# Performance work log

Hardware: AMD Instinct MI355X
Metric: run time of the kernel (lower is better)

The kernel has to match this reference:

```python
import jax, jax.numpy as jnp
import numpy as np
from jax.scipy.linalg import expm

DIM = 128
BF = 2          # branching_factor
H = 8           # num_heads
MAX_DEPTH = 12
PAD = BF + 1    # padding value used by pad_sequence in the torch module
N = 256         # number of positions


def setup_inputs() -> dict:
    key = jax.random.key(0)
    k1, k2 = jax.random.split(key)
    # raw _primitives parameter (the torch init applies softmax+cumsum to rand;
    # any values work for the math -- only the skew-hermitian part matters)
    prim = jax.random.uniform(k1, (BF * H + 1, DIM, DIM), dtype=jnp.float32)
    positions = jax.random.randint(k2, (N,), 0, BF ** MAX_DEPTH)  # node indices, >= 0
    return {"primitives_param": prim, "positions": positions}


def _path_words(positions):
    """Vectorized equivalent of create_paths + pad_sequence.

    For node index n the branch path is built by walking up the tree:
    branch = (n-1) % BF, parent = (n-1) // BF. Digits come out leaf->root,
    so we reverse the valid prefix and right-pad with PAD to MAX_DEPTH.
    """
    d = positions.astype(jnp.int32)
    digs = []
    for _ in range(MAX_DEPTH):
        valid = d > 0
        digs.append(jnp.where(valid, (d - 1) % BF, PAD))
        d = jnp.where(valid, (d - 1) // BF, 0)
    R = jnp.stack(digs, axis=1)            # (N, 12) leaf->root digits
    depth = jnp.sum(R != PAD, axis=1)       # path length per token
    idx = depth[:, None] - 1 - jnp.arange(MAX_DEPTH)[None, :]
    pw = jnp.take_along_axis(R, jnp.clip(idx, 0, MAX_DEPTH - 1), axis=1)
    pw = jnp.where(idx >= 0, pw, PAD)       # (N, 12) root->leaf, PAD-padded
    return pw, depth


def reference(primitives_param, positions):
    pw, depth = _path_words(positions)

    # ---- steps matrix (tree distance), mirrors the no_grad block ----
    pm = pw != PAD                                        # (N, 12)
    mask = pm[:, None, :] & pm[None, :, :]                # (N, N, 12)
    eq = pw[:, None, :] == pw[None, :, :]
    common = jnp.cumprod(eq.astype(jnp.int32), axis=-1).astype(bool) & mask
    cpl = common.sum(-1)                                  # common prefix length
    steps = depth[:, None] + depth[None, :] - 2 * cpl     # (N, N) int

    # ---- unitary primitives: expm of the skew(-hermitian, real) part ----
    skew = primitives_param - jnp.swapaxes(primitives_param, -1, -2)
    prims = expm(skew)                                    # (BF*H+1, DIM, DIM)
    sos = prims[-1]
    P = prims[:-1].reshape(BF, H, DIM, DIM)

    n_tok = pw.shape[0]
    maps = jnp.broadcast_to(jnp.eye(DIM, dtype=prims.dtype)[None, None],
                            (n_tok, H, DIM, DIM))
    sos_ptr = pw[:, 0] == -1                              # never true for pos>=0, kept for fidelity
    maps = jnp.where(sos_ptr[:, None, None, None], sos[None, None], maps)

    # fused gather-indexed scan over tree depth: instead of BF masked matmuls
    # per depth, gather each token's branch primitive and do one batched matmul.
    for d in range(MAX_DEPTH):
        sel = pw[:, d]                                    # (N,) in {0..BF-1} or PAD
        Pk = P[jnp.clip(sel, 0, BF - 1)]                  # (N, H, DIM, DIM)
        new = jnp.einsum('nhij,nhjk->nhik', maps, Pk)
        maps = jnp.where((sel < BF)[:, None, None, None], new, maps)

    return maps, steps
```

## Files before the change

### kernel.cpp

```cpp
#include <hip/hip_runtime.h>

typedef unsigned short ushort_t;
typedef unsigned int uint_t;
typedef __attribute__((ext_vector_type(8))) short bf16x8;
typedef __attribute__((ext_vector_type(4))) float f32x4;

#define NMAT 16
#define MSZ 16384
#define NTAB 126

__device__ __forceinline__ ushort_t f32_bf16(float f) {
  uint_t u = __builtin_bit_cast(uint_t, f);
  u += 0x7FFFu + ((u >> 16) & 1u);
  return (ushort_t)(u >> 16);
}

__device__ __forceinline__ float bf16_f32(ushort_t b) {
  uint_t u = ((uint_t)b) << 16;
  return __builtin_bit_cast(float, u);
}

__device__ __forceinline__ int swz(int r, int k) {
  return r * 128 + (((k >> 3) ^ (r & 7)) << 3) + (k & 7);
}

__device__ __forceinline__ int tab_off(int L) { return (1 << L) - 2; }

__device__ __forceinline__ void mm_frag(const ushort_t* U, const ushort_t* V,
                                        int r0, int c0, int quad, int l16,
                                        f32x4 (&acc)[4][4]) {
#pragma unroll
  for (int rt = 0; rt < 4; rt++)
#pragma unroll
    for (int ct = 0; ct < 4; ct++) {
      f32x4 z = {0.f, 0.f, 0.f, 0.f};
      acc[rt][ct] = z;
    }
#pragma unroll
  for (int kt = 0; kt < 4; kt++) {
    int k = kt * 32 + quad * 8;
    bf16x8 a[4], b[4];
#pragma unroll
    for (int rt = 0; rt < 4; rt++) a[rt] = *(const bf16x8*)(&U[swz(r0 + rt * 16 + l16, k)]);
#pragma unroll
    for (int ct = 0; ct < 4; ct++) b[ct] = *(const bf16x8*)(&V[swz(c0 + ct * 16 + l16, k)]);
#pragma unroll
    for (int rt = 0; rt < 4; rt++)
#pragma unroll
      for (int ct = 0; ct < 4; ct++)
        acc[rt][ct] = __builtin_amdgcn_mfma_f32_16x16x32_bf16(a[rt], b[ct], acc[rt][ct], 0, 0, 0);
  }
}

__device__ __forceinline__ void store_T(ushort_t* dst, const f32x4 (&acc)[4][4],
                                        int r0, int c0, int quad, int l16,
                                        float scale, float cdiag) {
#pragma unroll
  for (int rt = 0; rt < 4; rt++)
#pragma unroll
    for (int ct = 0; ct < 4; ct++) {
      int dr = r0 + rt * 16 + quad * 4, dc = c0 + ct * 16 + l16;
      float v[4];
#pragma unroll
      for (int i = 0; i < 4; i++) {
        v[i] = scale * acc[rt][ct][i];
        if (dr + i == dc) v[i] += cdiag;
      }
      uint2 pk;
      pk.x = (uint_t)f32_bf16(v[0]) | ((uint_t)f32_bf16(v[1]) << 16);
      pk.y = (uint_t)f32_bf16(v[2]) | ((uint_t)f32_bf16(v[3]) << 16);
      *(uint2*)(&dst[swz(dc, dr)]) = pk;
    }
}

__device__ __forceinline__ void set_ident(ushort_t* dst, int t, float c) {
  ushort_t cb = f32_bf16(c);
  for (int i = 0; i < 64; i++) {
    int e = i * 256 + t;
    int r = e >> 7, k = e & 127;
    dst[swz(r, k)] = (r == k) ? cb : (ushort_t)0;
  }
}

__global__ __launch_bounds__(256, 1) void expm1_kernel(const float* __restrict__ prim,
                                                       ushort_t* __restrict__ wsCS) {
  __shared__ ushort_t __align__(16) bufA[MSZ];
  __shared__ ushort_t __align__(16) bufB[MSZ];
  int kmat = blockIdx.x >> 1, which = blockIdx.x & 1;
  int t = threadIdx.x, wave = t >> 6, lane = t & 63;
  int quad = lane >> 4, l16 = lane & 15;
  int r0 = (wave >> 1) * 64, c0 = (wave & 1) * 64;
  const float* p = prim + kmat * MSZ;

  for (int i = 0; i < 64; i++) {
    int e = i * 256 + t;
    int r = e >> 7, c = e & 127;
    bufA[swz(r, c)] = f32_bf16((p[r * 128 + c] - p[c * 128 + r]) * 0.125f);
  }
  __syncthreads();

  f32x4 acc[4][4];
  mm_frag(bufA, bufA, r0, c0, quad, l16, acc);
  __syncthreads();
  store_T(bufB, acc, r0, c0, quad, l16, -1.f, 0.f);
  __syncthreads();

  uint2 yv[4][4];
#pragma unroll
  for (int rt = 0; rt < 4; rt++)
#pragma unroll
    for (int ct = 0; ct < 4; ct++) {
      int dr = r0 + rt * 16 + quad * 4, dc = c0 + ct * 16 + l16;
      yv[rt][ct] = *(const uint2*)(&bufB[swz(dc, dr)]);
    }

  mm_frag(bufB, bufB, r0, c0, quad, l16, acc);
  __syncthreads();
  store_T(bufB, acc, r0, c0, quad, l16, 1.f, 0.f);

  float coef[9];
  if (which == 0) {
    coef[0] = 1.f; coef[1] = 1.f / 2; coef[2] = 1.f / 24; coef[3] = 1.f / 720;
    coef[4] = 1.f / 40320; coef[5] = 1.f / 3628800.f; coef[6] = 1.f / 479001600.f;
    coef[7] = 1.f / 87178291200.f; coef[8] = 1.f / 20922789888000.f;
  } else {
    coef[0] = 1.f; coef[1] = 1.f / 6; coef[2] = 1.f / 120; coef[3] = 1.f / 5040;
    coef[4] = 1.f / 362880.f; coef[5] = 1.f / 39916800.f; coef[6] = 1.f / 6227020800.f;
    coef[7] = 1.f / 1307674368000.f; coef[8] = 1.f / 355687428096000.f;
  }

  set_ident(bufA, t, coef[8]);
  __syncthreads();

#pragma unroll
  for (int k = 3; k >= 0; k--) {
    mm_frag(bufB, bufA, r0, c0, quad, l16, acc);
    __syncthreads();
    float cd = coef[2 * k], cy = coef[2 * k + 1];
#pragma unroll
    for (int rt = 0; rt < 4; rt++)
#pragma unroll
      for (int ct = 0; ct < 4; ct++) {
        int dr = r0 + rt * 16 + quad * 4, dc = c0 + ct * 16 + l16;
        uint2 yp = yv[rt][ct];
        float y[4] = {bf16_f32((ushort_t)(yp.x & 0xffff)), bf16_f32((ushort_t)(yp.x >> 16)),
                      bf16_f32((ushort_t)(yp.y & 0xffff)), bf16_f32((ushort_t)(yp.y >> 16))};
        float v[4];
#pragma unroll
        for (int i = 0; i < 4; i++) {
          v[i] = acc[rt][ct][i] + cy * y[i];
          if (dr + i == dc) v[i] += cd;
        }
        uint2 pk;
        pk.x = (uint_t)f32_bf16(v[0]) | ((uint_t)f32_bf16(v[1]) << 16);
        pk.y = (uint_t)f32_bf16(v[2]) | ((uint_t)f32_bf16(v[3]) << 16);
        *(uint2*)(&bufA[swz(dc, dr)]) = pk;
      }
    __syncthreads();
  }
  ushort_t* dst = wsCS + (size_t)(which * NMAT + kmat) * MSZ;
  for (int i = 0; i < 8; i++) {
    int e = (i * 256 + t) * 8;
    int r = e >> 7, k = e & 127;
    *(uint4*)(dst + e) = *(const uint4*)(&bufA[swz(r, k)]);
  }
}

__global__ __launch_bounds__(256, 1) void expm2_kernel(
    const float* __restrict__ prim, const ushort_t* __restrict__ wsCS,
    ushort_t* __restrict__ TN, ushort_t* __restrict__ TT) {
  __shared__ ushort_t __align__(16) bufA[MSZ];
  __shared__ ushort_t __align__(16) bufB[MSZ];
  int kmat = blockIdx.x;
  int t = threadIdx.x, wave = t >> 6, lane = t & 63;
  int quad = lane >> 4, l16 = lane & 15;
  int r0 = (wave >> 1) * 64, c0 = (wave & 1) * 64;
  const float* p = prim + kmat * MSZ;
  const ushort_t* Cg = wsCS + (size_t)kmat * MSZ;
  const ushort_t* Sg = wsCS + (size_t)(NMAT + kmat) * MSZ;

  for (int i = 0; i < 64; i++) {
    int e = i * 256 + t;
    int r = e >> 7, c = e & 127;
    bufA[swz(r, c)] = f32_bf16((p[r * 128 + c] - p[c * 128 + r]) * 0.125f);
  }
  for (int i = 0; i < 8; i++) {
    int e = (i * 256 + t) * 8;
    int r = e >> 7, k = e & 127;
    *(uint4*)(&bufB[swz(r, k)]) = *(const uint4*)(Sg + e);
  }
  __syncthreads();

  f32x4 acc[4][4];
  mm_frag(bufA, bufB, r0, c0, quad, l16, acc);
  __syncthreads();
#pragma unroll
  for (int rt = 0; rt < 4; rt++)
#pragma unroll
    for (int ct = 0; ct < 4; ct++) {
      int dr = r0 + rt * 16 + quad * 4, dc = c0 + ct * 16 + l16;
      uint2 cp = *(const uint2*)(Cg + dc * 128 + dr);
      float cf[4] = {bf16_f32((ushort_t)(cp.x & 0xffff)), bf16_f32((ushort_t)(cp.x >> 16)),
                     bf16_f32((ushort_t)(cp.y & 0xffff)), bf16_f32((ushort_t)(cp.y >> 16))};
      uint2 en, et;
      en.x = (uint_t)f32_bf16(cf[0] - acc[rt][ct][0]) | ((uint_t)f32_bf16(cf[1] - acc[rt][ct][1]) << 16);
      en.y = (uint_t)f32_bf16(cf[2] - acc[rt][ct][2]) | ((uint_t)f32_bf16(cf[3] - acc[rt][ct][3]) << 16);
      et.x = (uint_t)f32_bf16(cf[0] + acc[rt][ct][0]) | ((uint_t)f32_bf16(cf[1] + acc[rt][ct][1]) << 16);
      et.y = (uint_t)f32_bf16(cf[2] + acc[rt][ct][2]) | ((uint_t)f32_bf16(cf[3] + acc[rt][ct][3]) << 16);
      *(uint2*)(&bufA[swz(dc, dr)]) = en;
      *(uint2*)(&bufB[swz(dc, dr)]) = et;
    }
  __syncthreads();

#pragma unroll 1
  for (int sq = 0; sq < 3; sq++) {
    mm_frag(bufA, bufB, r0, c0, quad, l16, acc);
    __syncthreads();
#pragma unroll
    for (int rt = 0; rt < 4; rt++)
#pragma unroll
      for (int ct = 0; ct < 4; ct++) {
        int dr = r0 + rt * 16 + quad * 4, dc = c0 + ct * 16 + l16;
        uint2 pk;
        pk.x = (uint_t)f32_bf16(acc[rt][ct][0]) | ((uint_t)f32_bf16(acc[rt][ct][1]) << 16);
        pk.y = (uint_t)f32_bf16(acc[rt][ct][2]) | ((uint_t)f32_bf16(acc[rt][ct][3]) << 16);
        *(uint2*)(&bufB[swz(dc, dr)]) = pk;
#pragma unroll
        for (int i = 0; i < 4; i++) bufA[swz(dr + i, dc)] = f32_bf16(acc[rt][ct][i]);
      }
    __syncthreads();
  }
  for (int i = 0; i < 8; i++) {
    int e = (i * 256 + t) * 8;
    int r = e >> 7, k = e & 127;
    *(uint4*)(TN + (size_t)kmat * MSZ + e) = *(const uint4*)(&bufA[swz(r, k)]);
    *(uint4*)(TT + (size_t)kmat * MSZ + e) = *(const uint4*)(&bufB[swz(r, k)]);
  }
}

__global__ __launch_bounds__(256) void table_kernel(ushort_t* __restrict__ TN,
                                                    ushort_t* __restrict__ TT, int mode) {
  int bx = blockIdx.x;
  int eA, eB, eO, h;
  if (mode == 0) {
    int c = bx >> 3; h = bx & 7;
    eA = c >> 1; eB = c & 1; eO = 2 + c;
  } else if (mode == 1) {
    if (bx < 64) {
      int c = bx >> 3; h = bx & 7;
      eA = 2 + (c >> 1); eB = c & 1; eO = 6 + c;
    } else {
      int c = (bx - 64) >> 3; h = (bx - 64) & 7;
      eA = 2 + (c >> 2); eB = 2 + (c & 3); eO = 14 + c;
    }
  } else {
    if (bx < 256) {
      int c = bx >> 3; h = bx & 7;
      eA = 2 + (c >> 3); eB = 6 + (c & 7); eO = 30 + c;
    } else {
      int c = (bx - 256) >> 3; h = (bx - 256) & 7;
      eA = 6 + (c >> 3); eB = 6 + (c & 7); eO = 62 + c;
    }
  }
  int t = threadIdx.x, wave = t >> 6, lane = t & 63;
  int quad = lane >> 4, l16 = lane & 15;
  int r0 = (wave >> 1) * 64, c0 = (wave & 1) * 64;
  const ushort_t* A = TN + ((size_t)eA * 8 + h) * MSZ;
  const ushort_t* B = TT + ((size_t)eB * 8 + h) * MSZ;
  ushort_t* oN = TN + ((size_t)eO * 8 + h) * MSZ;
  ushort_t* oT = TT + ((size_t)eO * 8 + h) * MSZ;

  f32x4 acc[4][4];
#pragma unroll
  for (int rt = 0; rt < 4; rt++)
#pragma unroll
    for (int ct = 0; ct < 4; ct++) {
      f32x4 z = {0.f, 0.f, 0.f, 0.f};
      acc[rt][ct] = z;
    }
#pragma unroll
  for (int kt = 0; kt < 4; kt++) {
    bf16x8 a[4], b[4];
#pragma unroll
    for (int rt = 0; rt < 4; rt++)
      a[rt] = *(const bf16x8*)(A + (r0 + rt * 16 + l16) * 128 + kt * 32 + quad * 8);
#pragma unroll
    for (int ct = 0; ct < 4; ct++)
      b[ct] = *(const bf16x8*)(B + (c0 + ct * 16 + l16) * 128 + kt * 32 + quad * 8);
#pragma unroll
    for (int rt = 0; rt < 4; rt++)
#pragma unroll
      for (int ct = 0; ct < 4; ct++)
        acc[rt][ct] = __builtin_amdgcn_mfma_f32_16x16x32_bf16(a[rt], b[ct], acc[rt][ct], 0, 0, 0);
  }
#pragma unroll
  for (int rt = 0; rt < 4; rt++)
#pragma unroll
    for (int ct = 0; ct < 4; ct++) {
      int dr = r0 + rt * 16 + quad * 4, dc = c0 + ct * 16 + l16;
      uint2 pk;
      pk.x = (uint_t)f32_bf16(acc[rt][ct][0]) | ((uint_t)f32_bf16(acc[rt][ct][1]) << 16);
      pk.y = (uint_t)f32_bf16(acc[rt][ct][2]) | ((uint_t)f32_bf16(acc[rt][ct][3]) << 16);
      *(uint2*)(oT + dc * 128 + dr) = pk;
#pragma unroll
      for (int i = 0; i < 4; i++) oN[(dr + i) * 128 + dc] = f32_bf16(acc[rt][ct][i]);
    }
}

__global__ void steps_kernel(const int* __restrict__ pos, float* __restrict__ os, int N) {
  int i = blockIdx.x, j = threadIdx.x;
  int mi = pos[i] + 1, mj = pos[j] + 1;
  int di = 31 - __builtin_clz((unsigned)mi);
  int dj = 31 - __builtin_clz((unsigned)mj);
  int tt = di < dj ? di : dj;
  unsigned x = (unsigned)((mi >> (di - tt)) ^ (mj >> (dj - tt)));
  int cpl = tt - (x ? (32 - __builtin_clz(x)) : 0);
  os[i * N + j] = (float)(di + dj - 2 * cpl);
}

__global__ __launch_bounds__(256) void maps_kernel(
    const ushort_t* __restrict__ TN, const ushort_t* __restrict__ TT,
    const int* __restrict__ positions, float* __restrict__ out) {
  int bx = blockIdx.x;
  int n = bx >> 3, h = bx & 7;
  int t = threadIdx.x, wave = t >> 6, lane = t & 63;
  int quad = lane >> 4, l16 = lane & 15;
  int m = positions[n] + 1;
  int depth = 31 - __builtin_clz((unsigned)m);
  float* ob = out + (size_t)(n * 8 + h) * MSZ;

  if (depth == 0) {
    for (int i = 0; i < 64; i++) {
      int e = i * 256 + t;
      int r = e >> 7, k = e & 127;
      ob[e] = (r == k) ? 1.0f : 0.0f;
    }
    return;
  }
  if (depth <= 6) {
    int c = m & ((1 << depth) - 1);
    const ushort_t* src = TN + ((size_t)(tab_off(depth) + c) * 8 + h) * MSZ;
    for (int i = 0; i < 8; i++) {
      int e = (i * 256 + t) * 8;
      bf16x8 v = *(const bf16x8*)(src + e);
      f32x4 lo = {bf16_f32((ushort_t)v[0]), bf16_f32((ushort_t)v[1]),
                  bf16_f32((ushort_t)v[2]), bf16_f32((ushort_t)v[3])};
      f32x4 hi = {bf16_f32((ushort_t)v[4]), bf16_f32((ushort_t)v[5]),
                  bf16_f32((ushort_t)v[6]), bf16_f32((ushort_t)v[7])};
      *(f32x4*)(ob + e) = lo;
      *(f32x4*)(ob + e + 4) = hi;
    }
    return;
  }

  int L0 = depth - 6;
  int c0v = (m >> 6) & ((1 << L0) - 1);
  int suf = m & 63;
  const ushort_t* U = TT + ((size_t)(62 + suf) * 8 + h) * MSZ;
  const ushort_t* V = TN + ((size_t)(tab_off(L0) + c0v) * 8 + h) * MSZ;

  int r0 = (wave >> 1) * 64, c0 = (wave & 1) * 64;
  f32x4 acc[4][4];
#pragma unroll
  for (int rt = 0; rt < 4; rt++)
#pragma unroll
    for (int ct = 0; ct < 4; ct++) {
      f32x4 z = {0.f, 0.f, 0.f, 0.f};
      acc[rt][ct] = z;
    }
#pragma unroll
  for (int kt = 0; kt < 4; kt++) {
    bf16x8 a[4], b[4];
#pragma unroll
    for (int rt = 0; rt < 4; rt++)
      a[rt] = *(const bf16x8*)(U + (r0 + rt * 16 + l16) * 128 + kt * 32 + quad * 8);
#pragma unroll
    for (int ct = 0; ct < 4; ct++)
      b[ct] = *(const bf16x8*)(V + (c0 + ct * 16 + l16) * 128 + kt * 32 + quad * 8);
#pragma unroll
    for (int rt = 0; rt < 4; rt++)
#pragma unroll
      for (int ct = 0; ct < 4; ct++)
        acc[rt][ct] = __builtin_amdgcn_mfma_f32_16x16x32_bf16(a[rt], b[ct], acc[rt][ct], 0, 0, 0);
  }
#pragma unroll
  for (int rt = 0; rt < 4; rt++)
#pragma unroll
    for (int ct = 0; ct < 4; ct++) {
      int dr = r0 + rt * 16 + quad * 4;
      int dc = c0 + ct * 16 + l16;
      *(f32x4*)(ob + dc * 128 + dr) = acc[rt][ct];
    }
}

extern "C" void kernel_launch(void* const* d_in, const int* in_sizes, int n_in,
                              void* d_out, int out_size, void* d_ws, size_t ws_size,
                              hipStream_t stream) {
  const float* prim = (const float*)d_in[0];
  const int* positions = (const int*)d_in[1];
  int N = in_sizes[1];
  float* out = (float*)d_out;

  ushort_t* wsCS = (ushort_t*)d_ws;
  ushort_t* TN = wsCS + (size_t)2 * NMAT * MSZ;
  ushort_t* TT = TN + (size_t)NTAB * 8 * MSZ;

  steps_kernel<<<N, N, 0, stream>>>(positions, out + (size_t)N * 8 * MSZ, N);
  expm1_kernel<<<2 * NMAT, 256, 0, stream>>>(prim, wsCS);
  expm2_kernel<<<NMAT, 256, 0, stream>>>(prim, wsCS, TN, TT);
  table_kernel<<<32, 256, 0, stream>>>(TN, TT, 0);
  table_kernel<<<192, 256, 0, stream>>>(TN, TT, 1);
  table_kernel<<<768, 256, 0, stream>>>(TN, TT, 2);
  maps_kernel<<<N * 8, 256, 0, stream>>>(TN, TT, positions, out);
}
```

Measured before the change: 242.2 us.

## Fuse steps into expm1, stage skew via LDS, restructure table build into two launches

The steps computation now runs as extra blocks of the expm1 launch. expm1 stages the input in LDS and builds the scaled skew matrix with coalesced reads instead of strided transposed global reads. It also writes the skew matrix to a workspace so expm2 can load it instead of recomputing it. The three table launches become two: tableA builds depth-2 and depth-3 entries inside one block through an LDS intermediate, and tableB builds the rest. Each table entry is now formed by two matmuls that write transposed-packed stores, rather than one matmul with scalar strided stores. The changes aim to cut launch count and uncoalesced memory traffic, at the cost of doubling the MFMA work in the table kernels.

```diff
diff --git a/kernel.cpp b/kernel.cpp
--- a/kernel.cpp
+++ b/kernel.cpp
@@ -26,16 +26,20 @@
 
 __device__ __forceinline__ int tab_off(int L) { return (1 << L) - 2; }
 
+__device__ __forceinline__ void mm_zero(f32x4 (&acc)[4][4]) {
+#pragma unroll
+  for (int rt = 0; rt < 4; rt++)
+#pragma unroll
+    for (int ct = 0; ct < 4; ct++) {
+      f32x4 z = {0.f, 0.f, 0.f, 0.f};
+      acc[rt][ct] = z;
+    }
+}
+
 __device__ __forceinline__ void mm_frag(const ushort_t* U, const ushort_t* V,
                                         int r0, int c0, int quad, int l16,
                                         f32x4 (&acc)[4][4]) {
-#pragma unroll
-  for (int rt = 0; rt < 4; rt++)
-#pragma unroll
-    for (int ct = 0; ct < 4; ct++) {
-      f32x4 z = {0.f, 0.f, 0.f, 0.f};
-      acc[rt][ct] = z;
-    }
+  mm_zero(acc);
 #pragma unroll
   for (int kt = 0; kt < 4; kt++) {
     int k = kt * 32 + quad * 8;
@@ -50,6 +54,80 @@
       for (int ct = 0; ct < 4; ct++)
         acc[rt][ct] = __builtin_amdgcn_mfma_f32_16x16x32_bf16(a[rt], b[ct], acc[rt][ct], 0, 0, 0);
   }
+}
+
+__device__ __forceinline__ void mm_gg(const ushort_t* gU, const ushort_t* gV,
+                                      int r0, int c0, int quad, int l16,
+                                      f32x4 (&acc)[4][4]) {
+  mm_zero(acc);
+#pragma unroll
+  for (int kt = 0; kt < 4; kt++) {
+    int k = kt * 32 + quad * 8;
+    bf16x8 a[4], b[4];
+#pragma unroll
+    for (int rt = 0; rt < 4; rt++) a[rt] = *(const bf16x8*)(gU + (r0 + rt * 16 + l16) * 128 + k);
+#pragma unroll
+    for (int ct = 0; ct < 4; ct++) b[ct] = *(const bf16x8*)(gV + (c0 + ct * 16 + l16) * 128 + k);
+#pragma unroll
+    for (int rt = 0; rt < 4; rt++)
+#pragma unroll
+      for (int ct = 0; ct < 4; ct++)
+        acc[rt][ct] = __builtin_amdgcn_mfma_f32_16x16x32_bf16(a[rt], b[ct], acc[rt][ct], 0, 0, 0);
+  }
+}
+
+__device__ __forceinline__ void mm_gl(const ushort_t* gU, const ushort_t* lV,
+                                      int r0, int c0, int quad, int l16,
+                                      f32x4 (&acc)[4][4]) {
+  mm_zero(acc);
+#pragma unroll
+  for (int kt = 0; kt < 4; kt++) {
+    int k = kt * 32 + quad * 8;
+    bf16x8 a[4], b[4];
+#pragma unroll
+    for (int rt = 0; rt < 4; rt++) a[rt] = *(const bf16x8*)(gU + (r0 + rt * 16 + l16) * 128 + k);
+#pragma unroll
+    for (int ct = 0; ct < 4; ct++) b[ct] = *(const bf16x8*)(&lV[swz(c0 + ct * 16 + l16, k)]);
+#pragma unroll
+    for (int rt = 0; rt < 4; rt++)
+#pragma unroll
+      for (int ct = 0; ct < 4; ct++)
+        acc[rt][ct] = __builtin_amdgcn_mfma_f32_16x16x32_bf16(a[rt], b[ct], acc[rt][ct], 0, 0, 0);
+  }
+}
+
+__device__ __forceinline__ void mm_lg(const ushort_t* lU, const ushort_t* gV,
+                                      int r0, int c0, int quad, int l16,
+                                      f32x4 (&acc)[4][4]) {
+  mm_zero(acc);
+#pragma unroll
+  for (int kt = 0; kt < 4; kt++) {
+    int k = kt * 32 + quad * 8;
+    bf16x8 a[4], b[4];
+#pragma unroll
+    for (int rt = 0; rt < 4; rt++) a[rt] = *(const bf16x8*)(&lU[swz(r0 + rt * 16 + l16, k)]);
+#pragma unroll
+    for (int ct = 0; ct < 4; ct++) b[ct] = *(const bf16x8*)(gV + (c0 + ct * 16 + l16) * 128 + k);
+#pragma unroll
+    for (int rt = 0; rt < 4; rt++)
+#pragma unroll
+      for (int ct = 0; ct < 4; ct++)
+        acc[rt][ct] = __builtin_amdgcn_mfma_f32_16x16x32_bf16(a[rt], b[ct], acc[rt][ct], 0, 0, 0);
+  }
+}
+
+__device__ __forceinline__ void store_pk_global(ushort_t* dst, const f32x4 (&acc)[4][4],
+                                                int r0, int c0, int quad, int l16) {
+#pragma unroll
+  for (int rt = 0; rt < 4; rt++)
+#pragma unroll
+    for (int ct = 0; ct < 4; ct++) {
+      int dr = r0 + rt * 16 + quad * 4, dc = c0 + ct * 16 + l16;
+      uint2 pk;
+      pk.x = (uint_t)f32_bf16(acc[rt][ct][0]) | ((uint_t)f32_bf16(acc[rt][ct][1]) << 16);
+      pk.y = (uint_t)f32_bf16(acc[rt][ct][2]) | ((uint_t)f32_bf16(acc[rt][ct][3]) << 16);
+      *(uint2*)(dst + dc * 128 + dr) = pk;
+    }
 }
 
 __device__ __forceinline__ void store_T(ushort_t* dst, const f32x4 (&acc)[4][4],
@@ -82,12 +160,31 @@
   }
 }
 
-__global__ __launch_bounds__(256, 1) void expm1_kernel(const float* __restrict__ prim,
-                                                       ushort_t* __restrict__ wsCS) {
-  __shared__ ushort_t __align__(16) bufA[MSZ];
-  __shared__ ushort_t __align__(16) bufB[MSZ];
-  int kmat = blockIdx.x >> 1, which = blockIdx.x & 1;
-  int t = threadIdx.x, wave = t >> 6, lane = t & 63;
+__global__ __launch_bounds__(256, 2) void expm1_kernel(
+    const float* __restrict__ prim, ushort_t* __restrict__ wsCS,
+    ushort_t* __restrict__ wsX, const int* __restrict__ pos,
+    float* __restrict__ os, int N) {
+  int bx = blockIdx.x;
+  int t = threadIdx.x;
+  if (bx >= 32) {
+    int i = bx - 32, j = t;
+    int mi = pos[i] + 1, mj = pos[j] + 1;
+    int di = 31 - __builtin_clz((unsigned)mi);
+    int dj = 31 - __builtin_clz((unsigned)mj);
+    int tt = di < dj ? di : dj;
+    unsigned x = (unsigned)((mi >> (di - tt)) ^ (mj >> (dj - tt)));
+    int cpl = tt - (x ? (32 - __builtin_clz(x)) : 0);
+    os[i * N + j] = (float)(di + dj - 2 * cpl);
+    return;
+  }
+
+  __shared__ ushort_t __align__(16) smem[2 * MSZ];
+  ushort_t* bufA = smem;
+  ushort_t* bufB = smem + MSZ;
+  float* pf = (float*)smem;
+
+  int kmat = bx >> 1, which = bx & 1;
+  int wave = t >> 6, lane = t & 63;
   int quad = lane >> 4, l16 = lane & 15;
   int r0 = (wave >> 1) * 64, c0 = (wave & 1) * 64;
   const float* p = prim + kmat * MSZ;
@@ -95,7 +192,30 @@
   for (int i = 0; i < 64; i++) {
     int e = i * 256 + t;
     int r = e >> 7, c = e & 127;
-    bufA[swz(r, c)] = f32_bf16((p[r * 128 + c] - p[c * 128 + r]) * 0.125f);
+    pf[r * 128 + (c ^ (r & 31))] = p[e];
+  }
+  __syncthreads();
+
+  ushort_t xr[64];
+#pragma unroll
+  for (int i = 0; i < 64; i++) {
+    int e = i * 256 + t;
+    int r = e >> 7, c = e & 127;
+    float a = pf[r * 128 + (c ^ (r & 31))];
+    float b = pf[c * 128 + (r ^ (c & 31))];
+    xr[i] = f32_bf16((a - b) * 0.125f);
+  }
+  __syncthreads();
+#pragma unroll
+  for (int i = 0; i < 64; i++) {
+    int e = i * 256 + t;
+    int r = e >> 7, c = e & 127;
+    bufA[swz(r, c)] = xr[i];
+  }
+  if (which == 0) {
+    ushort_t* xd = wsX + (size_t)kmat * MSZ;
+#pragma unroll
+    for (int i = 0; i < 64; i++) xd[i * 256 + t] = xr[i];
   }
   __syncthreads();
 
@@ -167,7 +287,7 @@
 }
 
 __global__ __launch_bounds__(256, 1) void expm2_kernel(
-    const float* __restrict__ prim, const ushort_t* __restrict__ wsCS,
+    const ushort_t* __restrict__ wsX, const ushort_t* __restrict__ wsCS,
     ushort_t* __restrict__ TN, ushort_t* __restrict__ TT) {
   __shared__ ushort_t __align__(16) bufA[MSZ];
   __shared__ ushort_t __align__(16) bufB[MSZ];
@@ -175,18 +295,14 @@
   int t = threadIdx.x, wave = t >> 6, lane = t & 63;
   int quad = lane >> 4, l16 = lane & 15;
   int r0 = (wave >> 1) * 64, c0 = (wave & 1) * 64;
-  const float* p = prim + kmat * MSZ;
+  const ushort_t* Xg = wsX + (size_t)kmat * MSZ;
   const ushort_t* Cg = wsCS + (size_t)kmat * MSZ;
   const ushort_t* Sg = wsCS + (size_t)(NMAT + kmat) * MSZ;
 
-  for (int i = 0; i < 64; i++) {
-    int e = i * 256 + t;
-    int r = e >> 7, c = e & 127;
-    bufA[swz(r, c)] = f32_bf16((p[r * 128 + c] - p[c * 128 + r]) * 0.125f);
-  }
   for (int i = 0; i < 8; i++) {
     int e = (i * 256 + t) * 8;
     int r = e >> 7, k = e & 127;
+    *(uint4*)(&bufA[swz(r, k)]) = *(const uint4*)(Xg + e);
     *(uint4*)(&bufB[swz(r, k)]) = *(const uint4*)(Sg + e);
   }
   __syncthreads();
@@ -238,84 +354,79 @@
   }
 }
 
-__global__ __launch_bounds__(256) void table_kernel(ushort_t* __restrict__ TN,
-                                                    ushort_t* __restrict__ TT, int mode) {
+__global__ __launch_bounds__(256, 2) void tableA_kernel(ushort_t* __restrict__ TN,
+                                                        ushort_t* __restrict__ TT) {
+  __shared__ ushort_t __align__(16) Mb[MSZ];
   int bx = blockIdx.x;
-  int eA, eB, eO, h;
-  if (mode == 0) {
-    int c = bx >> 3; h = bx & 7;
-    eA = c >> 1; eB = c & 1; eO = 2 + c;
-  } else if (mode == 1) {
-    if (bx < 64) {
-      int c = bx >> 3; h = bx & 7;
-      eA = 2 + (c >> 1); eB = c & 1; eO = 6 + c;
-    } else {
-      int c = (bx - 64) >> 3; h = (bx - 64) & 7;
-      eA = 2 + (c >> 2); eB = 2 + (c & 3); eO = 14 + c;
-    }
-  } else {
-    if (bx < 256) {
-      int c = bx >> 3; h = bx & 7;
-      eA = 2 + (c >> 3); eB = 6 + (c & 7); eO = 30 + c;
-    } else {
-      int c = (bx - 256) >> 3; h = (bx - 256) & 7;
-      eA = 6 + (c >> 3); eB = 6 + (c & 7); eO = 62 + c;
-    }
-  }
+  int idx = bx >> 3, h = bx & 7;
   int t = threadIdx.x, wave = t >> 6, lane = t & 63;
   int quad = lane >> 4, l16 = lane & 15;
   int r0 = (wave >> 1) * 64, c0 = (wave & 1) * 64;
-  const ushort_t* A = TN + ((size_t)eA * 8 + h) * MSZ;
-  const ushort_t* B = TT + ((size_t)eB * 8 + h) * MSZ;
+
+  int b0, bmid, blast, eO, nmid;
+  if (idx < 4) {
+    int c = idx;
+    b0 = c >> 1; blast = c & 1; bmid = 0; nmid = 0; eO = 2 + c;
+  } else {
+    int c = idx - 4;
+    b0 = c >> 2; bmid = (c >> 1) & 1; blast = c & 1; nmid = 1; eO = 6 + c;
+  }
+
+  {
+    const ushort_t* src = TN + ((size_t)b0 * 8 + h) * MSZ;
+#pragma unroll
+    for (int i = 0; i < 8; i++) {
+      int e = (i * 256 + t) * 8;
+      int r = e >> 7, k = e & 127;
+      *(uint4*)(&Mb[swz(r, k)]) = *(const uint4*)(src + e);
+    }
+  }
+  __syncthreads();
+
+  f32x4 acc[4][4];
+  if (nmid) {
+    const ushort_t* Pt = TT + ((size_t)bmid * 8 + h) * MSZ;
+    mm_gl(Pt, Mb, r0, c0, quad, l16, acc);
+    __syncthreads();
+    store_T(Mb, acc, r0, c0, quad, l16, 1.f, 0.f);
+    __syncthreads();
+  }
+
+  const ushort_t* Pt = TT + ((size_t)blast * 8 + h) * MSZ;
   ushort_t* oN = TN + ((size_t)eO * 8 + h) * MSZ;
   ushort_t* oT = TT + ((size_t)eO * 8 + h) * MSZ;
+  mm_gl(Pt, Mb, r0, c0, quad, l16, acc);
+  store_pk_global(oN, acc, r0, c0, quad, l16);
+  mm_lg(Mb, Pt, r0, c0, quad, l16, acc);
+  store_pk_global(oT, acc, r0, c0, quad, l16);
+}
+
+__global__ __launch_bounds__(256) void tableB_kernel(ushort_t* __restrict__ TN,
+                                                     ushort_t* __restrict__ TT) {
+  int bx = blockIdx.x;
+  int idx = bx >> 3, h = bx & 7;
+  int t = threadIdx.x, wave = t >> 6, lane = t & 63;
+  int quad = lane >> 4, l16 = lane & 15;
+  int r0 = (wave >> 1) * 64, c0 = (wave & 1) * 64;
+
+  int eA, eB, eO;
+  if (idx < 16) {
+    int c = idx;      eA = 2 + (c >> 2); eB = 2 + (c & 3); eO = 14 + c;
+  } else if (idx < 48) {
+    int c = idx - 16; eA = 2 + (c >> 3); eB = 6 + (c & 7); eO = 30 + c;
+  } else {
+    int c = idx - 48; eA = 6 + (c >> 3); eB = 6 + (c & 7); eO = 62 + c;
+  }
+  const ushort_t* An = TN + ((size_t)eA * 8 + h) * MSZ;
+  const ushort_t* Bt = TT + ((size_t)eB * 8 + h) * MSZ;
+  ushort_t* oN = TN + ((size_t)eO * 8 + h) * MSZ;
+  ushort_t* oT = TT + ((size_t)eO * 8 + h) * MSZ;
 
   f32x4 acc[4][4];
-#pragma unroll
-  for (int rt = 0; rt < 4; rt++)
-#pragma unroll
-    for (int ct = 0; ct < 4; ct++) {
-      f32x4 z = {0.f, 0.f, 0.f, 0.f};
-      acc[rt][ct] = z;
-    }
-#pragma unroll
-  for (int kt = 0; kt < 4; kt++) {
-    bf16x8 a[4], b[4];
-#pragma unroll
-    for (int rt = 0; rt < 4; rt++)
-      a[rt] = *(const bf16x8*)(A + (r0 + rt * 16 + l16) * 128 + kt * 32 + quad * 8);
-#pragma unroll
-    for (int ct = 0; ct < 4; ct++)
-      b[ct] = *(const bf16x8*)(B + (c0 + ct * 16 + l16) * 128 + kt * 32 + quad * 8);
-#pragma unroll
-    for (int rt = 0; rt < 4; rt++)
-#pragma unroll
-      for (int ct = 0; ct < 4; ct++)
-        acc[rt][ct] = __builtin_amdgcn_mfma_f32_16x16x32_bf16(a[rt], b[ct], acc[rt][ct], 0, 0, 0);
-  }
-#pragma unroll
-  for (int rt = 0; rt < 4; rt++)
-#pragma unroll
-    for (int ct = 0; ct < 4; ct++) {
-      int dr = r0 + rt * 16 + quad * 4, dc = c0 + ct * 16 + l16;
-      uint2 pk;
-      pk.x = (uint_t)f32_bf16(acc[rt][ct][0]) | ((uint_t)f32_bf16(acc[rt][ct][1]) << 16);
-      pk.y = (uint_t)f32_bf16(acc[rt][ct][2]) | ((uint_t)f32_bf16(acc[rt][ct][3]) << 16);
-      *(uint2*)(oT + dc * 128 + dr) = pk;
-#pragma unroll
-      for (int i = 0; i < 4; i++) oN[(dr + i) * 128 + dc] = f32_bf16(acc[rt][ct][i]);
-    }
-}
-
-__global__ void steps_kernel(const int* __restrict__ pos, float* __restrict__ os, int N) {
-  int i = blockIdx.x, j = threadIdx.x;
-  int mi = pos[i] + 1, mj = pos[j] + 1;
-  int di = 31 - __builtin_clz((unsigned)mi);
-  int dj = 31 - __builtin_clz((unsigned)mj);
-  int tt = di < dj ? di : dj;
-  unsigned x = (unsigned)((mi >> (di - tt)) ^ (mj >> (dj - tt)));
-  int cpl = tt - (x ? (32 - __builtin_clz(x)) : 0);
-  os[i * N + j] = (float)(di + dj - 2 * cpl);
+  mm_gg(Bt, An, r0, c0, quad, l16, acc);
+  store_pk_global(oN, acc, r0, c0, quad, l16);
+  mm_gg(An, Bt, r0, c0, quad, l16, acc);
+  store_pk_global(oT, acc, r0, c0, quad, l16);
 }
 
 __global__ __launch_bounds__(256) void maps_kernel(
@@ -361,28 +472,7 @@
 
   int r0 = (wave >> 1) * 64, c0 = (wave & 1) * 64;
   f32x4 acc[4][4];
-#pragma unroll
-  for (int rt = 0; rt < 4; rt++)
-#pragma unroll
-    for (int ct = 0; ct < 4; ct++) {
-      f32x4 z = {0.f, 0.f, 0.f, 0.f};
-      acc[rt][ct] = z;
-    }
-#pragma unroll
-  for (int kt = 0; kt < 4; kt++) {
-    bf16x8 a[4], b[4];
-#pragma unroll
-    for (int rt = 0; rt < 4; rt++)
-      a[rt] = *(const bf16x8*)(U + (r0 + rt * 16 + l16) * 128 + kt * 32 + quad * 8);
-#pragma unroll
-    for (int ct = 0; ct < 4; ct++)
-      b[ct] = *(const bf16x8*)(V + (c0 + ct * 16 + l16) * 128 + kt * 32 + quad * 8);
-#pragma unroll
-    for (int rt = 0; rt < 4; rt++)
-#pragma unroll
-      for (int ct = 0; ct < 4; ct++)
-        acc[rt][ct] = __builtin_amdgcn_mfma_f32_16x16x32_bf16(a[rt], b[ct], acc[rt][ct], 0, 0, 0);
-  }
+  mm_gg(U, V, r0, c0, quad, l16, acc);
 #pragma unroll
   for (int rt = 0; rt < 4; rt++)
 #pragma unroll
@@ -402,14 +492,14 @@
   float* out = (float*)d_out;
 
   ushort_t* wsCS = (ushort_t*)d_ws;
-  ushort_t* TN = wsCS + (size_t)2 * NMAT * MSZ;
+  ushort_t* wsX = wsCS + (size_t)2 * NMAT * MSZ;
+  ushort_t* TN = wsX + (size_t)NMAT * MSZ;
   ushort_t* TT = TN + (size_t)NTAB * 8 * MSZ;
 
-  steps_kernel<<<N, N, 0, stream>>>(positions, out + (size_t)N * 8 * MSZ, N);
-  expm1_kernel<<<2 * NMAT, 256, 0, stream>>>(prim, wsCS);
-  expm2_kernel<<<NMAT, 256, 0, stream>>>(prim, wsCS, TN, TT);
-  table_kernel<<<32, 256, 0, stream>>>(TN, TT, 0);
-  table_kernel<<<192, 256, 0, stream>>>(TN, TT, 1);
-  table_kernel<<<768, 256, 0, stream>>>(TN, TT, 2);
+  float* steps_out = out + (size_t)N * 8 * MSZ;
+  expm1_kernel<<<32 + N, 256, 0, stream>>>(prim, wsCS, wsX, positions, steps_out, N);
+  expm2_kernel<<<NMAT, 256, 0, stream>>>(wsX, wsCS, TN, TT);
+  tableA_kernel<<<96, 256, 0, stream>>>(TN, TT);
+  tableB_kernel<<<896, 256, 0, stream>>>(TN, TT);
   maps_kernel<<<N * 8, 256, 0, stream>>>(TN, TT, positions, out);
 }
```

Result: slower. 270.2 us (+11.6%).

## Shrink prefix-product table to depth 4 and chain up to two products per token

Applied to the files above, without the earlier changes.

The precomputed table of branch-primitive products now stops at depth 4 (30 entries) instead of depth 6 (126 entries). This removes the 768-block depth-6 table launch. The table stage becomes two kernels that compute each product directly as a pair of GEMMs for the normal and transposed layouts. The maps kernel now composes a deep path from up to three 4-level chunks. For depth 9-12 it does two matmuls per token-head, staging the intermediate in LDS. This trades table-building work for extra per-token matmuls and LDS use, plus a launch-bounds occupancy hint.

```diff
diff --git a/kernel.cpp b/kernel.cpp
--- a/kernel.cpp
+++ b/kernel.cpp
@@ -7,7 +7,7 @@
 
 #define NMAT 16
 #define MSZ 16384
-#define NTAB 126
+#define NTAB 30
 
 __device__ __forceinline__ ushort_t f32_bf16(float f) {
   uint_t u = __builtin_bit_cast(uint_t, f);
@@ -24,18 +24,24 @@
   return r * 128 + (((k >> 3) ^ (r & 7)) << 3) + (k & 7);
 }
 
-__device__ __forceinline__ int tab_off(int L) { return (1 << L) - 2; }
+__device__ __forceinline__ int tab_off(int L) {
+  return (L == 1) ? 0 : (L == 2) ? 2 : (L == 3) ? 6 : 14;
+}
+
+__device__ __forceinline__ void mm_zero(f32x4 (&acc)[4][4]) {
+#pragma unroll
+  for (int rt = 0; rt < 4; rt++)
+#pragma unroll
+    for (int ct = 0; ct < 4; ct++) {
+      f32x4 z = {0.f, 0.f, 0.f, 0.f};
+      acc[rt][ct] = z;
+    }
+}
 
 __device__ __forceinline__ void mm_frag(const ushort_t* U, const ushort_t* V,
                                         int r0, int c0, int quad, int l16,
                                         f32x4 (&acc)[4][4]) {
-#pragma unroll
-  for (int rt = 0; rt < 4; rt++)
-#pragma unroll
-    for (int ct = 0; ct < 4; ct++) {
-      f32x4 z = {0.f, 0.f, 0.f, 0.f};
-      acc[rt][ct] = z;
-    }
+  mm_zero(acc);
 #pragma unroll
   for (int kt = 0; kt < 4; kt++) {
     int k = kt * 32 + quad * 8;
@@ -50,6 +56,60 @@
       for (int ct = 0; ct < 4; ct++)
         acc[rt][ct] = __builtin_amdgcn_mfma_f32_16x16x32_bf16(a[rt], b[ct], acc[rt][ct], 0, 0, 0);
   }
+}
+
+__device__ __forceinline__ void mm_gg(const ushort_t* gU, const ushort_t* gV,
+                                      int r0, int c0, int quad, int l16,
+                                      f32x4 (&acc)[4][4]) {
+  mm_zero(acc);
+#pragma unroll
+  for (int kt = 0; kt < 4; kt++) {
+    int k = kt * 32 + quad * 8;
+    bf16x8 a[4], b[4];
+#pragma unroll
+    for (int rt = 0; rt < 4; rt++) a[rt] = *(const bf16x8*)(gU + (r0 + rt * 16 + l16) * 128 + k);
+#pragma unroll
+    for (int ct = 0; ct < 4; ct++) b[ct] = *(const bf16x8*)(gV + (c0 + ct * 16 + l16) * 128 + k);
+#pragma unroll
+    for (int rt = 0; rt < 4; rt++)
+#pragma unroll
+      for (int ct = 0; ct < 4; ct++)
+        acc[rt][ct] = __builtin_amdgcn_mfma_f32_16x16x32_bf16(a[rt], b[ct], acc[rt][ct], 0, 0, 0);
+  }
+}
+
+__device__ __forceinline__ void mm_gl(const ushort_t* gU, const ushort_t* lV,
+                                      int r0, int c0, int quad, int l16,
+                                      f32x4 (&acc)[4][4]) {
+  mm_zero(acc);
+#pragma unroll
+  for (int kt = 0; kt < 4; kt++) {
+    int k = kt * 32 + quad * 8;
+    bf16x8 a[4], b[4];
+#pragma unroll
+    for (int rt = 0; rt < 4; rt++) a[rt] = *(const bf16x8*)(gU + (r0 + rt * 16 + l16) * 128 + k);
+#pragma unroll
+    for (int ct = 0; ct < 4; ct++) b[ct] = *(const bf16x8*)(&lV[swz(c0 + ct * 16 + l16, k)]);
+#pragma unroll
+    for (int rt = 0; rt < 4; rt++)
+#pragma unroll
+      for (int ct = 0; ct < 4; ct++)
+        acc[rt][ct] = __builtin_amdgcn_mfma_f32_16x16x32_bf16(a[rt], b[ct], acc[rt][ct], 0, 0, 0);
+  }
+}
+
+__device__ __forceinline__ void store_pk_global(ushort_t* dst, const f32x4 (&acc)[4][4],
+                                                int r0, int c0, int quad, int l16) {
+#pragma unroll
+  for (int rt = 0; rt < 4; rt++)
+#pragma unroll
+    for (int ct = 0; ct < 4; ct++) {
+      int dr = r0 + rt * 16 + quad * 4, dc = c0 + ct * 16 + l16;
+      uint2 pk;
+      pk.x = (uint_t)f32_bf16(acc[rt][ct][0]) | ((uint_t)f32_bf16(acc[rt][ct][1]) << 16);
+      pk.y = (uint_t)f32_bf16(acc[rt][ct][2]) | ((uint_t)f32_bf16(acc[rt][ct][3]) << 16);
+      *(uint2*)(dst + dc * 128 + dr) = pk;
+    }
 }
 
 __device__ __forceinline__ void store_T(ushort_t* dst, const f32x4 (&acc)[4][4],
@@ -238,73 +298,52 @@
   }
 }
 
-__global__ __launch_bounds__(256) void table_kernel(ushort_t* __restrict__ TN,
-                                                    ushort_t* __restrict__ TT, int mode) {
+__global__ __launch_bounds__(256) void tableA_kernel(ushort_t* __restrict__ TN,
+                                                     ushort_t* __restrict__ TT) {
   int bx = blockIdx.x;
-  int eA, eB, eO, h;
-  if (mode == 0) {
-    int c = bx >> 3; h = bx & 7;
-    eA = c >> 1; eB = c & 1; eO = 2 + c;
-  } else if (mode == 1) {
-    if (bx < 64) {
-      int c = bx >> 3; h = bx & 7;
-      eA = 2 + (c >> 1); eB = c & 1; eO = 6 + c;
-    } else {
-      int c = (bx - 64) >> 3; h = (bx - 64) & 7;
-      eA = 2 + (c >> 2); eB = 2 + (c & 3); eO = 14 + c;
-    }
-  } else {
-    if (bx < 256) {
-      int c = bx >> 3; h = bx & 7;
-      eA = 2 + (c >> 3); eB = 6 + (c & 7); eO = 30 + c;
-    } else {
-      int c = (bx - 256) >> 3; h = (bx - 256) & 7;
-      eA = 6 + (c >> 3); eB = 6 + (c & 7); eO = 62 + c;
-    }
-  }
+  int c = bx >> 3, h = bx & 7;
   int t = threadIdx.x, wave = t >> 6, lane = t & 63;
   int quad = lane >> 4, l16 = lane & 15;
   int r0 = (wave >> 1) * 64, c0 = (wave & 1) * 64;
-  const ushort_t* A = TN + ((size_t)eA * 8 + h) * MSZ;
-  const ushort_t* B = TT + ((size_t)eB * 8 + h) * MSZ;
-  ushort_t* oN = TN + ((size_t)eO * 8 + h) * MSZ;
-  ushort_t* oT = TT + ((size_t)eO * 8 + h) * MSZ;
+
+  const ushort_t* An = TN + ((size_t)(c >> 1) * 8 + h) * MSZ;
+  const ushort_t* Bt = TT + ((size_t)(c & 1) * 8 + h) * MSZ;
+  ushort_t* oN = TN + ((size_t)(2 + c) * 8 + h) * MSZ;
+  ushort_t* oT = TT + ((size_t)(2 + c) * 8 + h) * MSZ;
 
   f32x4 acc[4][4];
-#pragma unroll
-  for (int rt = 0; rt < 4; rt++)
-#pragma unroll
-    for (int ct = 0; ct < 4; ct++) {
-      f32x4 z = {0.f, 0.f, 0.f, 0.f};
-      acc[rt][ct] = z;
-    }
-#pragma unroll
-  for (int kt = 0; kt < 4; kt++) {
-    bf16x8 a[4], b[4];
-#pragma unroll
-    for (int rt = 0; rt < 4; rt++)
-      a[rt] = *(const bf16x8*)(A + (r0 + rt * 16 + l16) * 128 + kt * 32 + quad * 8);
-#pragma unroll
-    for (int ct = 0; ct < 4; ct++)
-      b[ct] = *(const bf16x8*)(B + (c0 + ct * 16 + l16) * 128 + kt * 32 + quad * 8);
-#pragma unroll
-    for (int rt = 0; rt < 4; rt++)
-#pragma unroll
-      for (int ct = 0; ct < 4; ct++)
-        acc[rt][ct] = __builtin_amdgcn_mfma_f32_16x16x32_bf16(a[rt], b[ct], acc[rt][ct], 0, 0, 0);
-  }
-#pragma unroll
-  for (int rt = 0; rt < 4; rt++)
-#pragma unroll
-    for (int ct = 0; ct < 4; ct++) {
-      int dr = r0 + rt * 16 + quad * 4, dc = c0 + ct * 16 + l16;
-      uint2 pk;
-      pk.x = (uint_t)f32_bf16(acc[rt][ct][0]) | ((uint_t)f32_bf16(acc[rt][ct][1]) << 16);
-      pk.y = (uint_t)f32_bf16(acc[rt][ct][2]) | ((uint_t)f32_bf16(acc[rt][ct][3]) << 16);
-      *(uint2*)(oT + dc * 128 + dr) = pk;
-#pragma unroll
-      for (int i = 0; i < 4; i++) oN[(dr + i) * 128 + dc] = f32_bf16(acc[rt][ct][i]);
-    }
+  mm_gg(Bt, An, r0, c0, quad, l16, acc);
+  store_pk_global(oN, acc, r0, c0, quad, l16);
+  mm_gg(An, Bt, r0, c0, quad, l16, acc);
+  store_pk_global(oT, acc, r0, c0, quad, l16);
+}
+
+__global__ __launch_bounds__(256) void tableB_kernel(ushort_t* __restrict__ TN,
+                                                     ushort_t* __restrict__ TT) {
+  int bx = blockIdx.x;
+  int t = threadIdx.x, wave = t >> 6, lane = t & 63;
+  int quad = lane >> 4, l16 = lane & 15;
+  int r0 = (wave >> 1) * 64, c0 = (wave & 1) * 64;
+  f32x4 acc[4][4];
+
+  if (bx < 64) {
+    int c = bx >> 3, h = bx & 7;
+    const ushort_t* An = TN + ((size_t)(2 + (c >> 1)) * 8 + h) * MSZ;
+    const ushort_t* Bt = TT + ((size_t)(c & 1) * 8 + h) * MSZ;
+    ushort_t* oN = TN + ((size_t)(6 + c) * 8 + h) * MSZ;
+    mm_gg(Bt, An, r0, c0, quad, l16, acc);
+    store_pk_global(oN, acc, r0, c0, quad, l16);
+  } else {
+    int c = (bx - 64) >> 3, h = (bx - 64) & 7;
+    const ushort_t* An = TN + ((size_t)(2 + (c >> 2)) * 8 + h) * MSZ;
+    const ushort_t* Bt = TT + ((size_t)(2 + (c & 3)) * 8 + h) * MSZ;
+    ushort_t* oN = TN + ((size_t)(14 + c) * 8 + h) * MSZ;
+    ushort_t* oT = TT + ((size_t)(14 + c) * 8 + h) * MSZ;
+    mm_gg(Bt, An, r0, c0, quad, l16, acc);
+    store_pk_global(oN, acc, r0, c0, quad, l16);
+    mm_gg(An, Bt, r0, c0, quad, l16, acc);
+    store_pk_global(oT, acc, r0, c0, quad, l16);
+  }
 }
 
 __global__ void steps_kernel(const int* __restrict__ pos, float* __restrict__ os, int N) {
@@ -318,9 +357,10 @@
   os[i * N + j] = (float)(di + dj - 2 * cpl);
 }
 
-__global__ __launch_bounds__(256) void maps_kernel(
+__global__ __launch_bounds__(256, 4) void maps_kernel(
     const ushort_t* __restrict__ TN, const ushort_t* __restrict__ TT,
     const int* __restrict__ positions, float* __restrict__ out) {
+  __shared__ ushort_t __align__(16) Mb[MSZ];
   int bx = blockIdx.x;
   int n = bx >> 3, h = bx & 7;
   int t = threadIdx.x, wave = t >> 6, lane = t & 63;
@@ -337,7 +377,7 @@
     }
     return;
   }
-  if (depth <= 6) {
+  if (depth <= 4) {
     int c = m & ((1 << depth) - 1);
     const ushort_t* src = TN + ((size_t)(tab_off(depth) + c) * 8 + h) * MSZ;
     for (int i = 0; i < 8; i++) {
@@ -353,36 +393,24 @@
     return;
   }
 
-  int L0 = depth - 6;
-  int c0v = (m >> 6) & ((1 << L0) - 1);
-  int suf = m & 63;
-  const ushort_t* U = TT + ((size_t)(62 + suf) * 8 + h) * MSZ;
-  const ushort_t* V = TN + ((size_t)(tab_off(L0) + c0v) * 8 + h) * MSZ;
-
+  int K = (depth + 3) >> 2;
+  int L0 = depth - 4 * (K - 1);
+  int pre = (m >> (4 * (K - 1))) & ((1 << L0) - 1);
   int r0 = (wave >> 1) * 64, c0 = (wave & 1) * 64;
   f32x4 acc[4][4];
-#pragma unroll
-  for (int rt = 0; rt < 4; rt++)
-#pragma unroll
-    for (int ct = 0; ct < 4; ct++) {
-      f32x4 z = {0.f, 0.f, 0.f, 0.f};
-      acc[rt][ct] = z;
-    }
-#pragma unroll
-  for (int kt = 0; kt < 4; kt++) {
-    bf16x8 a[4], b[4];
-#pragma unroll
-    for (int rt = 0; rt < 4; rt++)
-      a[rt] = *(const bf16x8*)(U + (r0 + rt * 16 + l16) * 128 + kt * 32 + quad * 8);
-#pragma unroll
-    for (int ct = 0; ct < 4; ct++)
-      b[ct] = *(const bf16x8*)(V + (c0 + ct * 16 + l16) * 128 + kt * 32 + quad * 8);
-#pragma unroll
-    for (int rt = 0; rt < 4; rt++)
-#pragma unroll
-      for (int ct = 0; ct < 4; ct++)
-        acc[rt][ct] = __builtin_amdgcn_mfma_f32_16x16x32_bf16(a[rt], b[ct], acc[rt][ct], 0, 0, 0);
-  }
+
+  int c1 = (m >> (4 * (K - 2))) & 15;
+  mm_gg(TT + ((size_t)(14 + c1) * 8 + h) * MSZ,
+        TN + ((size_t)(tab_off(L0) + pre) * 8 + h) * MSZ,
+        r0, c0, quad, l16, acc);
+
+  if (K == 3) {
+    store_T(Mb, acc, r0, c0, quad, l16, 1.f, 0.f);
+    __syncthreads();
+    int c2 = m & 15;
+    mm_gl(TT + ((size_t)(14 + c2) * 8 + h) * MSZ, Mb, r0, c0, quad, l16, acc);
+  }
+
 #pragma unroll
   for (int rt = 0; rt < 4; rt++)
 #pragma unroll
@@ -408,8 +436,7 @@
   steps_kernel<<<N, N, 0, stream>>>(positions, out + (size_t)N * 8 * MSZ, N);
   expm1_kernel<<<2 * NMAT, 256, 0, stream>>>(prim, wsCS);
   expm2_kernel<<<NMAT, 256, 0, stream>>>(prim, wsCS, TN, TT);
-  table_kernel<<<32, 256, 0, stream>>>(TN, TT, 0);
-  table_kernel<<<192, 256, 0, stream>>>(TN, TT, 1);
-  table_kernel<<<768, 256, 0, stream>>>(TN, TT, 2);
+  tableA_kernel<<<32, 256, 0, stream>>>(TN, TT);
+  tableB_kernel<<<192, 256, 0, stream>>>(TN, TT);
   maps_kernel<<<N * 8, 256, 0, stream>>>(TN, TT, positions, out);
 }
```

New measurement: 249.5 us. +3.0%, slower.
